# Kernel optimization log

Hardware: AMD Instinct MI355X
Metric: run time of the kernel (lower is better)

Reference implementation:

```python
import jax, jax.numpy as jnp
import numpy as np
from jax import lax

S, B, IN, H, OUT = 2048, 4096, 1, 4, 1


def _lstm_layer(xs, W_ih, W_hh, b_ih, b_hh):
    # xs: (S, B, in). PyTorch gate order: i, f, g, o stacked along dim 0 of W (4H, in).
    gx = jnp.einsum('sbi,gi->sbg', xs, W_ih) + b_ih + b_hh  # (S, B, 4H)
    Bn = xs.shape[1]
    h0 = jnp.zeros((Bn, H), xs.dtype)
    c0 = jnp.zeros((Bn, H), xs.dtype)

    def step(carry, g_x):
        h, c = carry
        g = g_x + h @ W_hh.T  # (B, 4H)
        i, f, gg, o = jnp.split(g, 4, axis=-1)
        i = jax.nn.sigmoid(i)
        f = jax.nn.sigmoid(f)
        gg = jnp.tanh(gg)
        o = jax.nn.sigmoid(o)
        c = f * c + i * gg
        h = o * jnp.tanh(c)
        return (h, c), h

    _, hs = lax.scan(step, (h0, c0), gx)
    return hs  # (S, B, H)


def setup_inputs() -> dict:
    key = jax.random.key(0)
    ks = jax.random.split(key, 12)
    k = 1.0 / np.sqrt(H)
    u = lambda kk, shape: jax.random.uniform(kk, shape, jnp.float32, -k, k)
    return {
        'x': jax.random.normal(ks[0], (S, B, IN), jnp.float32),
        'W_ih0': u(ks[1], (4 * H, IN)),
        'W_hh0': u(ks[2], (4 * H, H)),
        'b_ih0': u(ks[3], (4 * H,)),
        'b_hh0': u(ks[4], (4 * H,)),
        'W_ih1': u(ks[5], (4 * H, H)),
        'W_hh1': u(ks[6], (4 * H, H)),
        'b_ih1': u(ks[7], (4 * H,)),
        'b_hh1': u(ks[8], (4 * H,)),
        'W_out': u(ks[9], (OUT, H)),
        'b_out': u(ks[10], (OUT,)),
    }


def reference(x, W_ih0, W_hh0, b_ih0, b_hh0, W_ih1, W_hh1, b_ih1, b_hh1, W_out, b_out):
    h1 = _lstm_layer(x, W_ih0, W_hh0, b_ih0, b_hh0)   # (S, B, H)
    h2 = _lstm_layer(h1, W_ih1, W_hh1, b_ih1, b_hh1)  # (S, B, H)
    out = jnp.einsum('sbh,oh->sbo', h2, W_out) + b_out  # (S, B, OUT)
    return out
```

## Files before the change

kernel.cpp:

```cpp
#include <hip/hip_runtime.h>
#include <math.h>

#define S_LEN 2048
#define B_N   4096
#define WARM  64
#define EMIT  124
#define NCH   16

typedef short short8 __attribute__((ext_vector_type(8)));
typedef float f32x16 __attribute__((ext_vector_type(16)));

__device__ __forceinline__ float hw_exp2(float x) { return __builtin_amdgcn_exp2f(x); }
__device__ __forceinline__ float hw_rcp(float x)  { return __builtin_amdgcn_rcpf(x); }

__device__ __forceinline__ unsigned f2u(float x) { return __float_as_uint(x); }
__device__ __forceinline__ float u2f(unsigned x) { return __uint_as_float(x); }
__device__ __forceinline__ float bhi(float x) { return u2f(f2u(x) & 0xFFFF0000u); }
__device__ __forceinline__ unsigned short btr(float x) { return (unsigned short)(f2u(x) >> 16); }
__device__ __forceinline__ unsigned short brne(float x) {
    unsigned u = f2u(x);
    return (unsigned short)((u + 0x7FFFu + ((u >> 16) & 1u)) >> 16);
}
__device__ __forceinline__ unsigned pack_hi2(float e, float o) {
    return __builtin_amdgcn_perm(f2u(o), f2u(e), 0x07060302u);
}
__device__ __forceinline__ unsigned pack_lo2(float e, float o) {
    float le = e - bhi(e), lo = o - bhi(o);
    return __builtin_amdgcn_perm(f2u(lo), f2u(le), 0x07060302u);
}

__global__ __launch_bounds__(256) void lstm2_kernel(
    const float* __restrict__ X,
    const float* __restrict__ Wih0, const float* __restrict__ Whh0,
    const float* __restrict__ bih0, const float* __restrict__ bhh0,
    const float* __restrict__ Wih1, const float* __restrict__ Whh1,
    const float* __restrict__ bih1, const float* __restrict__ bhh1,
    const float* __restrict__ Wout, const float* __restrict__ bOut,
    float* __restrict__ Y)
{
    const int tix   = threadIdx.x;
    const int wv    = tix >> 6;
    const int lane  = tix & 63;
    const int l32   = lane & 31;
    const int half  = lane >> 5;
    const int q     = blockIdx.x >> 5;
    const int chain = (blockIdx.x & 31) * 128 + wv * 32 + l32;

    const int t_start = EMIT * q;
    const int t_emit  = q ? t_start + WARM : 0;
    const int t_end   = t_start + EMIT + WARM;

    const float LOG2E = 1.4426950408889634f;
    const float TAU   = 2.8853900817779268f;
    const float KG    = -2.0f * TAU;

    const int rA   = l32;
    const int layA = (rA >> 2) & 1;
    const int giA  = rA >> 3;
    const int uuA  = rA & 3;
    const int ptgA = (giA == 0) ? 0 : (giA == 1) ? 2 : (giA == 2) ? 1 : 3;
    const int jA   = ptgA * 4 + uuA;
    const float sA = (giA == 1) ? TAU : -LOG2E;

    short8 a1, a2;
    #pragma unroll
    for (int e = 0; e < 8; ++e) {
        const int k = e & 3;
        float w;
        if (!half) w = layA ? Wih1[jA * 4 + k] : Whh0[jA * 4 + k];
        else       w = layA ? Whh1[jA * 4 + k] : 0.0f;
        w *= sA;
        a1[e] = (short)btr(w);
        a2[e] = (short)brne(w - bhi(w));
    }

    f32x16 biasC;
    float a0c[16];
    #pragma unroll
    for (int r = 0; r < 16; ++r) {
        const int gi = r >> 2, uu = r & 3;
        const int pg = (gi == 0) ? 0 : (gi == 1) ? 2 : (gi == 2) ? 1 : 3;
        const int jd = pg * 4 + uu;
        const float sr = (gi == 1) ? TAU : -LOG2E;
        biasC[r] = (half ? (bih1[jd] + bhh1[jd]) : (bih0[jd] + bhh0[jd])) * sr;
        a0c[r]   = half ? 0.0f : Wih0[jd] * sr;
    }
    const float wo0 = Wout[0], wo1 = Wout[1], wo2 = Wout[2], wo3 = Wout[3];
    const float bo  = bOut[0];

    int   bfi[4] = {0, 0, 0, 0};
    float Cc[4]  = {0.f, 0.f, 0.f, 0.f};

    auto STEP = [&](float x) -> float {
        union { int i[4]; short8 s; } bu;
        bu.i[0] = bfi[0]; bu.i[1] = bfi[1]; bu.i[2] = bfi[2]; bu.i[3] = bfi[3];
        f32x16 d = __builtin_amdgcn_mfma_f32_32x32x16_bf16(a1, bu.s, biasC, 0, 0, 0);
        d        = __builtin_amdgcn_mfma_f32_32x32x16_bf16(a2, bu.s, d,     0, 0, 0);

        float act[16];
        #pragma unroll
        for (int r = 0; r < 16; ++r)
            act[r] = hw_rcp(1.0f + hw_exp2(fmaf(x, a0c[r], d[r])));
        #pragma unroll
        for (int m = 0; m < 4; ++m)
            act[4 + m] = fmaf(KG, act[4 + m], TAU);

        float h[4];
        float y = bo;
        #pragma unroll
        for (int m = 0; m < 4; ++m) {
            Cc[m] = fmaf(act[8 + m], Cc[m], act[m] * act[4 + m]);
            float t = fmaf(-2.0f, hw_rcp(1.0f + hw_exp2(Cc[m])), 1.0f);
            h[m] = act[12 + m] * t;
        }
        y = fmaf(wo0, h[0], y);
        y = fmaf(wo1, h[1], y);
        y = fmaf(wo2, h[2], y);
        y = fmaf(wo3, h[3], y);

        bfi[0] = (int)pack_hi2(h[0], h[1]);
        bfi[1] = (int)pack_hi2(h[2], h[3]);
        bfi[2] = (int)pack_lo2(h[0], h[1]);
        bfi[3] = (int)pack_lo2(h[2], h[3]);
        return y;
    };

    (void)STEP(X[(size_t)t_start * B_N + chain]);
    if (half) {
        bfi[0] = 0; bfi[1] = 0; bfi[2] = 0; bfi[3] = 0;
        Cc[0] = 0.f; Cc[1] = 0.f; Cc[2] = 0.f; Cc[3] = 0.f;
    }

    float xb[4];
    #pragma unroll
    for (int u = 0; u < 4; ++u) xb[u] = X[(size_t)(t_start + 1 + u) * B_N + chain];

    for (int tt0 = t_start + 1; tt0 + 3 <= t_emit; tt0 += 4) {
        #pragma unroll
        for (int u = 0; u < 4; ++u) {
            float x = xb[u];
            xb[u] = X[(size_t)(tt0 + u + 4) * B_N + chain];
            (void)STEP(x);
        }
    }

    float ybuf[4];
    for (int tt0 = t_emit + 1; tt0 <= t_end - 11; tt0 += 4) {
        #pragma unroll
        for (int u = 0; u < 4; ++u) {
            float x = xb[u];
            xb[u] = X[(size_t)(tt0 + u + 4) * B_N + chain];
            ybuf[u] = STEP(x);
        }
        if (half) {
            #pragma unroll
            for (int u = 0; u < 4; ++u) Y[(size_t)(tt0 + u - 1) * B_N + chain] = ybuf[u];
        }
    }

    for (int tt0 = t_end - 7; tt0 <= t_end - 3; tt0 += 4) {
        #pragma unroll
        for (int u = 0; u < 4; ++u) {
            int tn = tt0 + u + 4; if (tn > S_LEN - 1) tn = S_LEN - 1;
            float x = xb[u];
            xb[u] = X[(size_t)tn * B_N + chain];
            ybuf[u] = STEP(x);
        }
        if (half) {
            #pragma unroll
            for (int u = 0; u < 4; ++u) Y[(size_t)(tt0 + u - 1) * B_N + chain] = ybuf[u];
        }
    }
}

extern "C" void kernel_launch(void* const* d_in, const int* in_sizes, int n_in,
                              void* d_out, int out_size, void* d_ws, size_t ws_size,
                              hipStream_t stream) {
    const float* X    = (const float*)d_in[0];
    const float* Wih0 = (const float*)d_in[1];
    const float* Whh0 = (const float*)d_in[2];
    const float* bih0 = (const float*)d_in[3];
    const float* bhh0 = (const float*)d_in[4];
    const float* Wih1 = (const float*)d_in[5];
    const float* Whh1 = (const float*)d_in[6];
    const float* bih1 = (const float*)d_in[7];
    const float* bhh1 = (const float*)d_in[8];
    const float* Wout = (const float*)d_in[9];
    const float* bOut = (const float*)d_in[10];
    float* Y = (float*)d_out;

    dim3 grid(NCH * 32), block(256);
    hipLaunchKernelGGL(lstm2_kernel, grid, block, 0, stream,
                       X, Wih0, Whh0, bih0, bhh0, Wih1, Whh1, bih1, bhh1, Wout, bOut, Y);
}
```

Before: 126.3 us.

## Interleave two independent chains per wave to hide recurrent step latency

Each wave now advances two independent batch-chain groups (A and B) in lockstep, interleaving their MFMA and transcendental sequences. The grid is halved to match. The intent is to give the scheduler independent work to fill the dependent MFMA-to-activation latency of the serial recurrence. In exchange it doubles register pressure and halves the number of waves, which lowers occupancy (512 to 256 blocks of 4 waves on a 256-CU part).

```diff
diff --git a/kernel.cpp b/kernel.cpp
--- a/kernel.cpp
+++ b/kernel.cpp
@@ -43,8 +43,10 @@
     const int lane  = tix & 63;
     const int l32   = lane & 31;
     const int half  = lane >> 5;
-    const int q     = blockIdx.x >> 5;
-    const int chain = (blockIdx.x & 31) * 128 + wv * 32 + l32;
+    const int q     = blockIdx.x >> 4;
+    const int cg    = blockIdx.x & 15;
+    const int chain0 = cg * 256 + wv * 64 + l32;
+    const int chain1 = chain0 + 32;
 
     const int t_start = EMIT * q;
     const int t_emit  = q ? t_start + WARM : 0;
@@ -88,10 +90,10 @@
     const float wo0 = Wout[0], wo1 = Wout[1], wo2 = Wout[2], wo3 = Wout[3];
     const float bo  = bOut[0];
 
-    int   bfi[4] = {0, 0, 0, 0};
-    float Cc[4]  = {0.f, 0.f, 0.f, 0.f};
-
-    auto STEP = [&](float x) -> float {
+    int   bfA[4] = {0,0,0,0}, bfB[4] = {0,0,0,0};
+    float CcA[4] = {0,0,0,0}, CcB[4] = {0,0,0,0};
+
+    auto STEP = [&](float x, int bfi[4], float Cc[4]) -> float {
         union { int i[4]; short8 s; } bu;
         bu.i[0] = bfi[0]; bu.i[1] = bfi[1]; bu.i[2] = bfi[2]; bu.i[3] = bfi[3];
         f32x16 d = __builtin_amdgcn_mfma_f32_32x32x16_bf16(a1, bu.s, biasC, 0, 0, 0);
@@ -125,36 +127,49 @@
         return y;
     };
 
-    (void)STEP(X[(size_t)t_start * B_N + chain]);
+    (void)STEP(X[(size_t)t_start * B_N + chain0], bfA, CcA);
+    (void)STEP(X[(size_t)t_start * B_N + chain1], bfB, CcB);
     if (half) {
-        bfi[0] = 0; bfi[1] = 0; bfi[2] = 0; bfi[3] = 0;
-        Cc[0] = 0.f; Cc[1] = 0.f; Cc[2] = 0.f; Cc[3] = 0.f;
-    }
-
-    float xb[4];
+        bfA[0]=0; bfA[1]=0; bfA[2]=0; bfA[3]=0;
+        bfB[0]=0; bfB[1]=0; bfB[2]=0; bfB[3]=0;
+        CcA[0]=0.f; CcA[1]=0.f; CcA[2]=0.f; CcA[3]=0.f;
+        CcB[0]=0.f; CcB[1]=0.f; CcB[2]=0.f; CcB[3]=0.f;
+    }
+
+    float xbA[4], xbB[4];
     #pragma unroll
-    for (int u = 0; u < 4; ++u) xb[u] = X[(size_t)(t_start + 1 + u) * B_N + chain];
+    for (int u = 0; u < 4; ++u) {
+        xbA[u] = X[(size_t)(t_start + 1 + u) * B_N + chain0];
+        xbB[u] = X[(size_t)(t_start + 1 + u) * B_N + chain1];
+    }
 
     for (int tt0 = t_start + 1; tt0 + 3 <= t_emit; tt0 += 4) {
         #pragma unroll
         for (int u = 0; u < 4; ++u) {
-            float x = xb[u];
-            xb[u] = X[(size_t)(tt0 + u + 4) * B_N + chain];
-            (void)STEP(x);
-        }
-    }
-
-    float ybuf[4];
+            float xa = xbA[u], xb = xbB[u];
+            xbA[u] = X[(size_t)(tt0 + u + 4) * B_N + chain0];
+            xbB[u] = X[(size_t)(tt0 + u + 4) * B_N + chain1];
+            (void)STEP(xa, bfA, CcA);
+            (void)STEP(xb, bfB, CcB);
+        }
+    }
+
+    float ybA[4], ybB[4];
     for (int tt0 = t_emit + 1; tt0 <= t_end - 11; tt0 += 4) {
         #pragma unroll
         for (int u = 0; u < 4; ++u) {
-            float x = xb[u];
-            xb[u] = X[(size_t)(tt0 + u + 4) * B_N + chain];
-            ybuf[u] = STEP(x);
+            float xa = xbA[u], xb = xbB[u];
+            xbA[u] = X[(size_t)(tt0 + u + 4) * B_N + chain0];
+            xbB[u] = X[(size_t)(tt0 + u + 4) * B_N + chain1];
+            ybA[u] = STEP(xa, bfA, CcA);
+            ybB[u] = STEP(xb, bfB, CcB);
         }
         if (half) {
             #pragma unroll
-            for (int u = 0; u < 4; ++u) Y[(size_t)(tt0 + u - 1) * B_N + chain] = ybuf[u];
+            for (int u = 0; u < 4; ++u) {
+                Y[(size_t)(tt0 + u - 1) * B_N + chain0] = ybA[u];
+                Y[(size_t)(tt0 + u - 1) * B_N + chain1] = ybB[u];
+            }
         }
     }
 
@@ -162,13 +177,18 @@
         #pragma unroll
         for (int u = 0; u < 4; ++u) {
             int tn = tt0 + u + 4; if (tn > S_LEN - 1) tn = S_LEN - 1;
-            float x = xb[u];
-            xb[u] = X[(size_t)tn * B_N + chain];
-            ybuf[u] = STEP(x);
+            float xa = xbA[u], xb = xbB[u];
+            xbA[u] = X[(size_t)tn * B_N + chain0];
+            xbB[u] = X[(size_t)tn * B_N + chain1];
+            ybA[u] = STEP(xa, bfA, CcA);
+            ybB[u] = STEP(xb, bfB, CcB);
         }
         if (half) {
             #pragma unroll
-            for (int u = 0; u < 4; ++u) Y[(size_t)(tt0 + u - 1) * B_N + chain] = ybuf[u];
+            for (int u = 0; u < 4; ++u) {
+                Y[(size_t)(tt0 + u - 1) * B_N + chain0] = ybA[u];
+                Y[(size_t)(tt0 + u - 1) * B_N + chain1] = ybB[u];
+            }
         }
     }
 }
@@ -189,7 +209,7 @@
     const float* bOut = (const float*)d_in[10];
     float* Y = (float*)d_out;
 
-    dim3 grid(NCH * 32), block(256);
+    dim3 grid(NCH * 16), block(256);
     hipLaunchKernelGGL(lstm2_kernel, grid, block, 0, stream,
                        X, Wih0, Whh0, bih0, bhh0, Wih1, Whh1, bih1, bhh1, Wout, bOut, Y);
 }
```

Result: slower. 128.8 us (+2.0%).
